# Kernel optimization log

Measured on AMD Instinct MI355X. Metric: run time of the kernel, lower is better.

## Reference

```python
import jax, jax.numpy as jnp
import numpy as np

N_HEAD = 12

def setup_inputs() -> dict:
    key = jax.random.key(0)
    ks = jax.random.split(key, 5)
    B, T, C = 4, 2048, 768
    scale = 0.02
    return {
        "x": jax.random.normal(ks[0], (B, T, C), dtype=jnp.float32),
        "W_attn": jax.random.normal(ks[1], (C, 3 * C), dtype=jnp.float32) * scale,
        "b_attn": jax.random.normal(ks[2], (3 * C,), dtype=jnp.float32) * scale,
        "W_proj": jax.random.normal(ks[3], (C, C), dtype=jnp.float32) * scale,
        "b_proj": jax.random.normal(ks[4], (C,), dtype=jnp.float32) * scale,
    }

def reference(x, W_attn, b_attn, W_proj, b_proj):
    B, T, C = x.shape
    H = N_HEAD
    D = C // H  # head dim
    qkv = x @ W_attn + b_attn  # [B,T,3C]
    q, k, v = jnp.split(qkv, 3, axis=-1)
    # [B,H,T,D]
    q = q.reshape(B, T, H, D).transpose(0, 2, 1, 3)
    k = k.reshape(B, T, H, D).transpose(0, 2, 1, 3)
    v = v.reshape(B, T, H, D).transpose(0, 2, 1, 3)
    scores = jnp.einsum('bhqd,bhkd->bhqk', q, k) / jnp.sqrt(jnp.float32(D))
    causal = jnp.tril(jnp.ones((T, T), dtype=bool))
    scores = jnp.where(causal[None, None, :, :], scores, jnp.float32(-jnp.inf))
    attn = jax.nn.softmax(scores, axis=-1)
    out = jnp.einsum('bhqk,bhkd->bhqd', attn, v)  # [B,H,T,D]
    out = out.transpose(0, 2, 1, 3).reshape(B, T, C)
    return out @ W_proj + b_proj
```

## Files before the change

kernel.cpp:

```cpp
#include <hip/hip_runtime.h>

typedef float f32x4 __attribute__((ext_vector_type(4)));
typedef __bf16 bf16x8 __attribute__((ext_vector_type(8)));
typedef unsigned short u16x8 __attribute__((ext_vector_type(8)));
typedef unsigned short u16x4 __attribute__((ext_vector_type(4)));

#define MFMA16(a, b, c) __builtin_amdgcn_mfma_f32_16x16x32_bf16((a), (b), (c), 0, 0, 0)

__device__ __forceinline__ unsigned short f2bf(float f) {
    __bf16 h = (__bf16)f;
    union { __bf16 h; unsigned short u; } c; c.h = h;
    return c.u;
}

__device__ __forceinline__ void gload_lds16(const unsigned short* g, unsigned short* l) {
    __builtin_amdgcn_global_load_lds(
        (const __attribute__((address_space(1))) unsigned int*)g,
        (__attribute__((address_space(3))) unsigned int*)l, 16, 0, 0);
}

__global__ void k_convert_bf16(const float* __restrict__ in,
                               unsigned short* __restrict__ out, int n) {
    int i = (blockIdx.x * 256 + threadIdx.x) * 4;
    if (i + 3 < n) {
        float4 v = *reinterpret_cast<const float4*>(in + i);
        ushort4 o;
        o.x = f2bf(v.x); o.y = f2bf(v.y); o.z = f2bf(v.z); o.w = f2bf(v.w);
        *reinterpret_cast<ushort4*>(out + i) = o;
    }
}

__global__ void k_transpose_bf16(const float* __restrict__ in,
                                 unsigned short* __restrict__ out, int R, int C) {
    __shared__ unsigned short tile[32][33];
    int bx = blockIdx.x * 32;
    int by = blockIdx.y * 32;
    int tx = threadIdx.x;
    int ty = threadIdx.y;
    #pragma unroll
    for (int i = ty; i < 32; i += 8)
        tile[i][tx] = f2bf(in[(size_t)(by + i) * C + bx + tx]);
    __syncthreads();
    #pragma unroll
    for (int i = ty; i < 32; i += 8)
        out[(size_t)(bx + i) * R + by + tx] = tile[tx][i];
}

template<int EPI>
__global__ __launch_bounds__(512) void k_gemm_bt(
    const unsigned short* __restrict__ A,
    const unsigned short* __restrict__ Bt,
    const float* __restrict__ bias,
    unsigned short* __restrict__ Qo,
    unsigned short* __restrict__ Ko,
    unsigned short* __restrict__ Vto,
    float* __restrict__ Co,
    int K)
{
    __shared__ unsigned short SM[(256 + 128) * 64];
    unsigned short* As = SM;
    unsigned short* Bs = SM + 256 * 64;
    const int nwg = gridDim.x * gridDim.y;
    const int bid0 = blockIdx.y * gridDim.x + blockIdx.x;
    const int logical = (bid0 & 7) * (nwg >> 3) + (bid0 >> 3);
    const int bm = logical / gridDim.x;
    const int bn = logical % gridDim.x;
    const int tid = threadIdx.x;
    const int w = tid >> 6, l = tid & 63;
    const int wm = w >> 1, wn = w & 1;
    const int ln = l & 15, kb = l >> 4;

    f32x4 acc[4][4];
    #pragma unroll
    for (int i = 0; i < 4; ++i)
        #pragma unroll
        for (int j = 0; j < 4; ++j)
            #pragma unroll
            for (int r = 0; r < 4; ++r) acc[i][j][r] = 0.f;

    const unsigned short* Ab = A + (size_t)(bm * 256) * K;
    const unsigned short* Bb = Bt + (size_t)(bn * 128) * K;

    const int srow = tid >> 3;
    const int sslot = tid & 7;
    const int csw = (sslot ^ (srow & 7)) * 8;

    for (int k0 = 0; k0 < K; k0 += 64) {
        #pragma unroll
        for (int j = 0; j < 4; ++j) {
            const int r = j * 64 + srow;
            gload_lds16(&Ab[(size_t)r * K + k0 + csw], &As[r * 64 + sslot * 8]);
        }
        #pragma unroll
        for (int j = 0; j < 2; ++j) {
            const int r = j * 64 + srow;
            gload_lds16(&Bb[(size_t)r * K + k0 + csw], &Bs[r * 64 + sslot * 8]);
        }
        __syncthreads();
        #pragma unroll
        for (int kh = 0; kh < 2; ++kh) {
            bf16x8 af[4], bfr[4];
            #pragma unroll
            for (int mt = 0; mt < 4; ++mt) {
                const int row = wm * 64 + mt * 16 + ln;
                const int slot = ((kh << 2) | kb) ^ (row & 7);
                af[mt] = *reinterpret_cast<const bf16x8*>(&As[row * 64 + slot * 8]);
            }
            #pragma unroll
            for (int nt = 0; nt < 4; ++nt) {
                const int row = wn * 64 + nt * 16 + ln;
                const int slot = ((kh << 2) | kb) ^ (row & 7);
                bfr[nt] = *reinterpret_cast<const bf16x8*>(&Bs[row * 64 + slot * 8]);
            }
            #pragma unroll
            for (int mt = 0; mt < 4; ++mt)
                #pragma unroll
                for (int nt = 0; nt < 4; ++nt)
                    acc[mt][nt] = MFMA16(af[mt], bfr[nt], acc[mt][nt]);
        }
        __syncthreads();
    }

    const float SC = 0.1803368801111204f;

    if (EPI == 0 && bn >= 12) {
        unsigned short* Ts = SM;
        const int cl_w = wn * 64;
        #pragma unroll
        for (int hh2 = 0; hh2 < 2; ++hh2) {
            if ((wm >> 1) == hh2) {
                #pragma unroll
                for (int mt = 0; mt < 4; ++mt) {
                    #pragma unroll
                    for (int nt = 0; nt < 4; ++nt) {
                        const int cl = cl_w + nt * 16 + ln;
                        const float bv = bias[bn * 128 + cl];
                        #pragma unroll
                        for (int r = 0; r < 4; ++r) {
                            const int rl = (wm & 1) * 64 + mt * 16 + kb * 4 + r;
                            const int pos = cl * 128 + ((((rl >> 3) ^ (cl & 7)) << 3) | (rl & 7));
                            Ts[pos] = f2bf(acc[mt][nt][r] + bv);
                        }
                    }
                }
            }
            __syncthreads();
            {
                const int cl = tid >> 2;
                const int col = bn * 128 + cl;
                const int cc = col - 1536;
                const int hh = cc >> 6, dd = cc & 63;
                #pragma unroll
                for (int j8 = 0; j8 < 4; ++j8) {
                    const int rb = (tid & 3) * 4 + j8;
                    u16x8 val = *reinterpret_cast<const u16x8*>(&Ts[cl * 128 + ((rb ^ (cl & 7)) << 3)]);
                    const int tg = bm * 256 + hh2 * 128 + rb * 8;
                    const int bb = tg >> 11;
                    const int tloc = tg & 2047;
                    const int grp = tloc & ~31;
                    const int jj = (tloc >> 3) & 3;
                    const int tlo = grp + 8 * ((2 * jj) & 3) + 4 * (jj >> 1);
                    const int thi = grp + 8 * ((2 * jj + 1) & 3) + 4 * (jj >> 1);
                    unsigned short* basep = &Vto[((size_t)((bb * 12 + hh) * 64 + dd)) * 2048];
                    *reinterpret_cast<u16x4*>(basep + tlo) =
                        __builtin_shufflevector(val, val, 0, 1, 2, 3);
                    *reinterpret_cast<u16x4*>(basep + thi) =
                        __builtin_shufflevector(val, val, 4, 5, 6, 7);
                }
            }
            __syncthreads();
        }
        return;
    }

    #pragma unroll
    for (int mt = 0; mt < 4; ++mt) {
        #pragma unroll
        for (int nt = 0; nt < 4; ++nt) {
            const int col = bn * 128 + wn * 64 + nt * 16 + ln;
            #pragma unroll
            for (int r = 0; r < 4; ++r) {
                const int row = bm * 256 + wm * 64 + mt * 16 + kb * 4 + r;
                float v = acc[mt][nt][r] + bias[col];
                if (EPI == 0) {
                    int cc = col >= 768 ? col - 768 : col;
                    int h = cc >> 6, d = cc & 63;
                    int b = row >> 11, t = row & 2047;
                    if (col < 768)
                        Qo[((size_t)((b * 12 + h) * 2048 + t)) * 64 + d] = f2bf(v * SC);
                    else
                        Ko[((size_t)((b * 12 + h) * 2048 + t)) * 64 + d] = f2bf(v);
                } else {
                    Co[(size_t)row * 768 + col] = v;
                }
            }
        }
    }
}

__global__ __launch_bounds__(256) void k_attn(
    const unsigned short* __restrict__ Q,
    const unsigned short* __restrict__ Kk,
    const unsigned short* __restrict__ Vt,
    unsigned short* __restrict__ Oo)
{
    __shared__ unsigned short SMEM[4 * 4096];
    const int bid0 = blockIdx.x;
    const int xcd = bid0 & 7;
    const int loc = bid0 >> 3;
    const int qb = 15 - (loc / 6);
    const int bh = xcd * 6 + (loc % 6);
    const int tid = threadIdx.x;
    const int w = tid >> 6, l = tid & 63;
    const int ln = l & 15, kb = l >> 4;
    const int kbq = kb * 4;
    const int b = bh / 12, h = bh - b * 12;
    const int q0w = qb * 128 + w * 32;

    const unsigned short* Qb = Q + (size_t)bh * 2048 * 64;
    const unsigned short* Kb = Kk + (size_t)bh * 2048 * 64;
    const unsigned short* Vb = Vt + (size_t)bh * 64 * 2048;

    bf16x8 qf[2][2];
    #pragma unroll
    for (int qn = 0; qn < 2; ++qn) {
        const unsigned short* qr = &Qb[(size_t)(q0w + qn * 16 + ln) * 64 + kb * 8];
        qf[qn][0] = *reinterpret_cast<const bf16x8*>(qr);
        qf[qn][1] = *reinterpret_cast<const bf16x8*>(qr + 32);
    }

    bf16x8 vones;
    #pragma unroll
    for (int e = 0; e < 8; ++e) vones[e] = (__bf16)1.0f;
    const f32x4 fzero = {0.f, 0.f, 0.f, 0.f};

    f32x4 oaccT[2][4];
    f32x4 den[2];
    #pragma unroll
    for (int qn = 0; qn < 2; ++qn) {
        #pragma unroll
        for (int r = 0; r < 4; ++r) den[qn][r] = 0.f;
        #pragma unroll
        for (int dt = 0; dt < 4; ++dt)
            #pragma unroll
            for (int r = 0; r < 4; ++r) oaccT[qn][dt][r] = 0.f;
    }

    const int lb = ln & 7;
    const int aR0 = ln * 64 + (kb ^ lb) * 8;
    const int aR1 = ln * 64 + ((4 | kb) ^ lb) * 8;

    const int srow = tid >> 3;
    const int sslot = tid & 7;
    const int csw = (sslot ^ (srow & 7)) * 8;
    const int ntile = 2 * qb + 2;
    const int lastkt = (q0w + 31) >> 6;

    #define STAGE(kt_, buf_)                                                        \
        {                                                                           \
            const int kb_ = (kt_) * 64;                                             \
            _Pragma("unroll")                                                       \
            for (int j = 0; j < 2; ++j) {                                           \
                const int r = j * 32 + srow;                                        \
                gload_lds16(&Kb[(size_t)(kb_ + r) * 64 + csw],                      \
                            &SMEM[(buf_) * 4096 + r * 64 + sslot * 8]);             \
                gload_lds16(&Vb[(size_t)r * 2048 + kb_ + csw],                      \
                            &SMEM[8192 + (buf_) * 4096 + r * 64 + sslot * 8]);      \
            }                                                                       \
        }

    #define COMPUTE(kt_, BUF)                                                       \
        if ((kt_) <= lastkt) {                                                      \
            bf16x8 kf[4][2];                                                        \
            _Pragma("unroll")                                                       \
            for (int km = 0; km < 4; ++km) {                                        \
                kf[km][0] = *reinterpret_cast<const bf16x8*>(                       \
                    &SMEM[(BUF) * 4096 + km * 1024 + aR0]);                         \
                kf[km][1] = *reinterpret_cast<const bf16x8*>(                       \
                    &SMEM[(BUF) * 4096 + km * 1024 + aR1]);                         \
            }                                                                       \
            f32x4 st[4][2];                                                         \
            _Pragma("unroll")                                                       \
            for (int km = 0; km < 4; ++km)                                          \
                _Pragma("unroll")                                                   \
                for (int qn = 0; qn < 2; ++qn) {                                    \
                    st[km][qn] = MFMA16(kf[km][0], qf[qn][0], fzero);               \
                    st[km][qn] = MFMA16(kf[km][1], qf[qn][1], st[km][qn]);          \
                }                                                                   \
            bf16x8 vf[4][2];                                                        \
            _Pragma("unroll")                                                       \
            for (int dt = 0; dt < 4; ++dt) {                                        \
                vf[dt][0] = *reinterpret_cast<const bf16x8*>(                       \
                    &SMEM[8192 + (BUF) * 4096 + dt * 1024 + aR0]);                  \
                vf[dt][1] = *reinterpret_cast<const bf16x8*>(                       \
                    &SMEM[8192 + (BUF) * 4096 + dt * 1024 + aR1]);                  \
            }                                                                       \
            if ((kt_) == lastkt) {                                                  \
                const int kbase_ = (kt_) * 64;                                      \
                _Pragma("unroll")                                                   \
                for (int qn = 0; qn < 2; ++qn) {                                    \
                    const int qrow = q0w + qn * 16 + ln;                            \
                    _Pragma("unroll")                                               \
                    for (int km = 0; km < 4; ++km)                                  \
                        _Pragma("unroll")                                           \
                        for (int r = 0; r < 4; ++r) {                               \
                            float sv = st[km][qn][r];                               \
                            const int key = kbase_ + km * 16 + kbq + r;             \
                            sv = (key <= qrow) ? sv : -1e30f;                       \
                            st[km][qn][r] = __builtin_amdgcn_exp2f(sv);             \
                        }                                                           \
                }                                                                   \
            } else {                                                                \
                _Pragma("unroll")                                                   \
                for (int qn = 0; qn < 2; ++qn)                                      \
                    _Pragma("unroll")                                               \
                    for (int km = 0; km < 4; ++km)                                  \
                        _Pragma("unroll")                                           \
                        for (int r = 0; r < 4; ++r)                                 \
                            st[km][qn][r] =                                         \
                                __builtin_amdgcn_exp2f(st[km][qn][r]);              \
            }                                                                       \
            bf16x8 pa[2][2];                                                        \
            _Pragma("unroll")                                                       \
            for (int qn = 0; qn < 2; ++qn)                                          \
                _Pragma("unroll")                                                   \
                for (int kh = 0; kh < 2; ++kh) {                                    \
                    bf16x8 t;                                                       \
                    _Pragma("unroll")                                               \
                    for (int r = 0; r < 4; ++r) {                                   \
                        t[r]     = (__bf16)st[2 * kh][qn][r];                       \
                        t[r + 4] = (__bf16)st[2 * kh + 1][qn][r];                   \
                    }                                                               \
                    pa[qn][kh] = t;                                                 \
                }                                                                   \
            _Pragma("unroll")                                                       \
            for (int qn = 0; qn < 2; ++qn) {                                        \
                _Pragma("unroll")                                                   \
                for (int dt = 0; dt < 4; ++dt) {                                    \
                    oaccT[qn][dt] = MFMA16(pa[qn][0], vf[dt][0], oaccT[qn][dt]);    \
                    oaccT[qn][dt] = MFMA16(pa[qn][1], vf[dt][1], oaccT[qn][dt]);    \
                }                                                                   \
                den[qn] = MFMA16(pa[qn][0], vones, den[qn]);                        \
                den[qn] = MFMA16(pa[qn][1], vones, den[qn]);                        \
            }                                                                       \
        }

    STAGE(0, 0);

    for (int s = 0; s <= qb; ++s) {
        const int ktA = 2 * s;
        const int ktB = 2 * s + 1;
        __syncthreads();
        STAGE(ktB, 1);
        COMPUTE(ktA, 0);
        __syncthreads();
        if (s < qb) STAGE(ktA + 2, 0);
        COMPUTE(ktB, 1);
    }

    #pragma unroll
    for (int qn = 0; qn < 2; ++qn) {
        #pragma unroll
        for (int r = 0; r < 4; ++r) {
            const float inv = 1.0f / den[qn][r];
            const int t = q0w + qn * 16 + kbq + r;
            #pragma unroll
            for (int dt = 0; dt < 4; ++dt)
                Oo[((size_t)(b * 2048 + t)) * 768 + h * 64 + dt * 16 + ln] =
                    f2bf(oaccT[qn][dt][r] * inv);
        }
    }
    #undef STAGE
    #undef COMPUTE
}

extern "C" void kernel_launch(void* const* d_in, const int* in_sizes, int n_in,
                              void* d_out, int out_size, void* d_ws, size_t ws_size,
                              hipStream_t stream) {
    const float* x      = (const float*)d_in[0];
    const float* W_attn = (const float*)d_in[1];
    const float* b_attn = (const float*)d_in[2];
    const float* W_proj = (const float*)d_in[3];
    const float* b_proj = (const float*)d_in[4];
    float* out = (float*)d_out;

    char* ws = (char*)d_ws;
    const size_t SZ_X  = (size_t)8192 * 768 * 2;
    const size_t SZ_WA = (size_t)2304 * 768 * 2;
    const size_t SZ_WP = (size_t)768 * 768 * 2;
    const size_t SZ_T  = (size_t)8192 * 768 * 2;

    unsigned short* x_bf = (unsigned short*)(ws);
    unsigned short* wa_t = (unsigned short*)(ws + SZ_X);
    unsigned short* wp_t = (unsigned short*)(ws + SZ_X + SZ_WA);
    unsigned short* Qb   = (unsigned short*)(ws + SZ_X + SZ_WA + SZ_WP);
    unsigned short* Kb   = (unsigned short*)(ws + SZ_X + SZ_WA + SZ_WP + SZ_T);
    unsigned short* Vtb  = (unsigned short*)(ws + SZ_X + SZ_WA + SZ_WP + 2 * SZ_T);
    unsigned short* attn_o = x_bf;

    k_convert_bf16<<<6144, 256, 0, stream>>>(x, x_bf, 8192 * 768);
    dim3 tb(32, 8);
    k_transpose_bf16<<<dim3(2304 / 32, 768 / 32), tb, 0, stream>>>(W_attn, wa_t, 768, 2304);
    k_transpose_bf16<<<dim3(768 / 32, 768 / 32), tb, 0, stream>>>(W_proj, wp_t, 768, 768);
    k_gemm_bt<0><<<dim3(18, 32), 512, 0, stream>>>(x_bf, wa_t, b_attn, Qb, Kb, Vtb, nullptr, 768);
    k_attn<<<768, 256, 0, stream>>>(Qb, Kb, Vtb, attn_o);
    k_gemm_bt<1><<<dim3(6, 32), 512, 0, stream>>>(attn_o, wp_t, b_proj, nullptr, nullptr, nullptr, out, 768);
}
```

Before: 121.0 us.

## Triple-buffer QKV GEMM pipeline and split projection GEMM into smaller tiles

The QKV GEMM now uses a three-stage LDS ring with K-step 32. It issues loads two steps ahead and waits on partial vmcnt, so global loads overlap the MFMA work instead of being fenced by a full sync every iteration. The output projection becomes its own kernel with 128x128 tiles and 256 threads over a 6x64 grid, which doubles the number of workgroups for the small GEMM. This costs more LDS per QKV block and adds hand-written waitcnt and barrier scheduling that must match the load counts exactly.

```diff
diff --git a/kernel.cpp b/kernel.cpp
--- a/kernel.cpp
+++ b/kernel.cpp
@@ -46,20 +46,16 @@
         out[(size_t)(bx + i) * R + by + tx] = tile[tx][i];
 }
 
-template<int EPI>
-__global__ __launch_bounds__(512) void k_gemm_bt(
+__global__ __launch_bounds__(512) void k_gemm_qkv(
     const unsigned short* __restrict__ A,
     const unsigned short* __restrict__ Bt,
     const float* __restrict__ bias,
     unsigned short* __restrict__ Qo,
     unsigned short* __restrict__ Ko,
     unsigned short* __restrict__ Vto,
-    float* __restrict__ Co,
     int K)
 {
-    __shared__ unsigned short SM[(256 + 128) * 64];
-    unsigned short* As = SM;
-    unsigned short* Bs = SM + 256 * 64;
+    __shared__ unsigned short SM[3 * 8192 + 3 * 4096];
     const int nwg = gridDim.x * gridDim.y;
     const int bid0 = blockIdx.y * gridDim.x + blockIdx.x;
     const int logical = (bid0 & 7) * (nwg >> 3) + (bid0 >> 3);
@@ -81,49 +77,60 @@
     const unsigned short* Ab = A + (size_t)(bm * 256) * K;
     const unsigned short* Bb = Bt + (size_t)(bn * 128) * K;
 
-    const int srow = tid >> 3;
-    const int sslot = tid & 7;
-    const int csw = (sslot ^ (srow & 7)) * 8;
-
-    for (int k0 = 0; k0 < K; k0 += 64) {
-        #pragma unroll
-        for (int j = 0; j < 4; ++j) {
-            const int r = j * 64 + srow;
-            gload_lds16(&Ab[(size_t)r * K + k0 + csw], &As[r * 64 + sslot * 8]);
-        }
-        #pragma unroll
-        for (int j = 0; j < 2; ++j) {
-            const int r = j * 64 + srow;
-            gload_lds16(&Bb[(size_t)r * K + k0 + csw], &Bs[r * 64 + sslot * 8]);
-        }
-        __syncthreads();
-        #pragma unroll
-        for (int kh = 0; kh < 2; ++kh) {
-            bf16x8 af[4], bfr[4];
-            #pragma unroll
-            for (int mt = 0; mt < 4; ++mt) {
-                const int row = wm * 64 + mt * 16 + ln;
-                const int slot = ((kh << 2) | kb) ^ (row & 7);
-                af[mt] = *reinterpret_cast<const bf16x8*>(&As[row * 64 + slot * 8]);
-            }
-            #pragma unroll
-            for (int nt = 0; nt < 4; ++nt) {
-                const int row = wn * 64 + nt * 16 + ln;
-                const int slot = ((kh << 2) | kb) ^ (row & 7);
-                bfr[nt] = *reinterpret_cast<const bf16x8*>(&Bs[row * 64 + slot * 8]);
-            }
-            #pragma unroll
-            for (int mt = 0; mt < 4; ++mt)
-                #pragma unroll
-                for (int nt = 0; nt < 4; ++nt)
-                    acc[mt][nt] = MFMA16(af[mt], bfr[nt], acc[mt][nt]);
-        }
-        __syncthreads();
-    }
+    const int srow = tid >> 2;
+    const int sslot = tid & 3;
+    const int scs = (sslot ^ ((srow >> 1) & 3)) * 8;
+    const int slot8 = (kb ^ ((ln >> 1) & 3)) * 8;
+    const int aOff = (wm * 64 + ln) * 32 + slot8;
+    const int bOff = 24576 + (wn * 64 + ln) * 32 + slot8;
+
+    #define QSTAGE(t_, buf_)                                                        \
+        {                                                                           \
+            const int k0_ = (t_) * 32;                                              \
+            gload_lds16(&Ab[(size_t)srow * K + k0_ + scs],                          \
+                        &SM[(buf_) * 8192 + srow * 32 + sslot * 8]);                \
+            gload_lds16(&Ab[(size_t)(128 + srow) * K + k0_ + scs],                  \
+                        &SM[(buf_) * 8192 + (128 + srow) * 32 + sslot * 8]);        \
+            gload_lds16(&Bb[(size_t)srow * K + k0_ + scs],                          \
+                        &SM[24576 + (buf_) * 4096 + srow * 32 + sslot * 8]);        \
+        }
+
+    #define QSTEP(t_, BUF_, NBUF_)                                                  \
+        {                                                                           \
+            if ((t_) < 23) { asm volatile("s_waitcnt vmcnt(3)" ::: "memory"); }     \
+            else           { asm volatile("s_waitcnt vmcnt(0)" ::: "memory"); }     \
+            __builtin_amdgcn_sched_barrier(0);                                      \
+            __builtin_amdgcn_s_barrier();                                           \
+            if ((t_) + 2 < 24) QSTAGE((t_) + 2, NBUF_);                             \
+            bf16x8 af[4], bfr[4];                                                   \
+            _Pragma("unroll")                                                       \
+            for (int mt = 0; mt < 4; ++mt)                                          \
+                af[mt] = *reinterpret_cast<const bf16x8*>(                          \
+                    &SM[(BUF_) * 8192 + mt * 512 + aOff]);                          \
+            _Pragma("unroll")                                                       \
+            for (int nt = 0; nt < 4; ++nt)                                          \
+                bfr[nt] = *reinterpret_cast<const bf16x8*>(                         \
+                    &SM[(BUF_) * 4096 + nt * 512 + bOff]);                          \
+            _Pragma("unroll")                                                       \
+            for (int mt = 0; mt < 4; ++mt)                                          \
+                _Pragma("unroll")                                                   \
+                for (int nt = 0; nt < 4; ++nt)                                      \
+                    acc[mt][nt] = MFMA16(af[mt], bfr[nt], acc[mt][nt]);             \
+        }
+
+    QSTAGE(0, 0);
+    QSTAGE(1, 1);
+    #pragma unroll
+    for (int s = 0; s < 8; ++s) {
+        QSTEP(3 * s,     0, 2);
+        QSTEP(3 * s + 1, 1, 0);
+        QSTEP(3 * s + 2, 2, 1);
+    }
+    __syncthreads();
 
     const float SC = 0.1803368801111204f;
 
-    if (EPI == 0 && bn >= 12) {
+    if (bn >= 12) {
         unsigned short* Ts = SM;
         const int cl_w = wn * 64;
         #pragma unroll
@@ -182,17 +189,101 @@
             for (int r = 0; r < 4; ++r) {
                 const int row = bm * 256 + wm * 64 + mt * 16 + kb * 4 + r;
                 float v = acc[mt][nt][r] + bias[col];
-                if (EPI == 0) {
-                    int cc = col >= 768 ? col - 768 : col;
-                    int h = cc >> 6, d = cc & 63;
-                    int b = row >> 11, t = row & 2047;
-                    if (col < 768)
-                        Qo[((size_t)((b * 12 + h) * 2048 + t)) * 64 + d] = f2bf(v * SC);
-                    else
-                        Ko[((size_t)((b * 12 + h) * 2048 + t)) * 64 + d] = f2bf(v);
-                } else {
-                    Co[(size_t)row * 768 + col] = v;
-                }
+                int cc = col >= 768 ? col - 768 : col;
+                int h = cc >> 6, d = cc & 63;
+                int b = row >> 11, t = row & 2047;
+                if (col < 768)
+                    Qo[((size_t)((b * 12 + h) * 2048 + t)) * 64 + d] = f2bf(v * SC);
+                else
+                    Ko[((size_t)((b * 12 + h) * 2048 + t)) * 64 + d] = f2bf(v);
+            }
+        }
+    }
+    #undef QSTAGE
+    #undef QSTEP
+}
+
+__global__ __launch_bounds__(256) void k_gemm_proj(
+    const unsigned short* __restrict__ A,
+    const unsigned short* __restrict__ Bt,
+    const float* __restrict__ bias,
+    float* __restrict__ Co,
+    int K)
+{
+    constexpr int BM = 128;
+    __shared__ unsigned short SM[(BM + 128) * 64];
+    unsigned short* As = SM;
+    unsigned short* Bs = SM + BM * 64;
+    const int nwg = gridDim.x * gridDim.y;
+    const int bid0 = blockIdx.y * gridDim.x + blockIdx.x;
+    const int logical = (bid0 & 7) * (nwg >> 3) + (bid0 >> 3);
+    const int bm = logical / gridDim.x;
+    const int bn = logical % gridDim.x;
+    const int tid = threadIdx.x;
+    const int w = tid >> 6, l = tid & 63;
+    const int wm = w >> 1, wn = w & 1;
+    const int ln = l & 15, kb = l >> 4;
+
+    f32x4 acc[4][4];
+    #pragma unroll
+    for (int i = 0; i < 4; ++i)
+        #pragma unroll
+        for (int j = 0; j < 4; ++j)
+            #pragma unroll
+            for (int r = 0; r < 4; ++r) acc[i][j][r] = 0.f;
+
+    const unsigned short* Ab = A + (size_t)(bm * BM) * K;
+    const unsigned short* Bb = Bt + (size_t)(bn * 128) * K;
+
+    const int srow = tid >> 3;
+    const int sslot = tid & 7;
+    const int csw = (sslot ^ (srow & 7)) * 8;
+
+    for (int k0 = 0; k0 < K; k0 += 64) {
+        #pragma unroll
+        for (int j = 0; j < 4; ++j) {
+            const int r = j * 32 + srow;
+            gload_lds16(&Ab[(size_t)r * K + k0 + csw], &As[r * 64 + sslot * 8]);
+        }
+        #pragma unroll
+        for (int j = 0; j < 4; ++j) {
+            const int r = j * 32 + srow;
+            gload_lds16(&Bb[(size_t)r * K + k0 + csw], &Bs[r * 64 + sslot * 8]);
+        }
+        __syncthreads();
+        #pragma unroll
+        for (int kh = 0; kh < 2; ++kh) {
+            bf16x8 af[4], bfr[4];
+            #pragma unroll
+            for (int mt = 0; mt < 4; ++mt) {
+                const int row = wm * 64 + mt * 16 + ln;
+                const int slot = ((kh << 2) | kb) ^ (row & 7);
+                af[mt] = *reinterpret_cast<const bf16x8*>(&As[row * 64 + slot * 8]);
+            }
+            #pragma unroll
+            for (int nt = 0; nt < 4; ++nt) {
+                const int row = wn * 64 + nt * 16 + ln;
+                const int slot = ((kh << 2) | kb) ^ (row & 7);
+                bfr[nt] = *reinterpret_cast<const bf16x8*>(&Bs[row * 64 + slot * 8]);
+            }
+            #pragma unroll
+            for (int mt = 0; mt < 4; ++mt)
+                #pragma unroll
+                for (int nt = 0; nt < 4; ++nt)
+                    acc[mt][nt] = MFMA16(af[mt], bfr[nt], acc[mt][nt]);
+        }
+        __syncthreads();
+    }
+
+    #pragma unroll
+    for (int mt = 0; mt < 4; ++mt) {
+        #pragma unroll
+        for (int nt = 0; nt < 4; ++nt) {
+            const int col = bn * 128 + wn * 64 + nt * 16 + ln;
+            #pragma unroll
+            for (int r = 0; r < 4; ++r) {
+                const int row = bm * BM + wm * 64 + mt * 16 + kb * 4 + r;
+                Co[(size_t)row * 768 + col] = acc[mt][nt][r] + bias[col];
             }
         }
     }
@@ -253,7 +344,6 @@
     const int srow = tid >> 3;
     const int sslot = tid & 7;
     const int csw = (sslot ^ (srow & 7)) * 8;
-    const int ntile = 2 * qb + 2;
     const int lastkt = (q0w + 31) >> 6;
 
     #define STAGE(kt_, buf_)                                                        \
@@ -402,7 +492,7 @@
     dim3 tb(32, 8);
     k_transpose_bf16<<<dim3(2304 / 32, 768 / 32), tb, 0, stream>>>(W_attn, wa_t, 768, 2304);
     k_transpose_bf16<<<dim3(768 / 32, 768 / 32), tb, 0, stream>>>(W_proj, wp_t, 768, 768);
-    k_gemm_bt<0><<<dim3(18, 32), 512, 0, stream>>>(x_bf, wa_t, b_attn, Qb, Kb, Vtb, nullptr, 768);
+    k_gemm_qkv<<<dim3(18, 32), 512, 0, stream>>>(x_bf, wa_t, b_attn, Qb, Kb, Vtb, 768);
     k_attn<<<768, 256, 0, stream>>>(Qb, Kb, Vtb, attn_o);
-    k_gemm_bt<1><<<dim3(6, 32), 512, 0, stream>>>(attn_o, wp_t, b_proj, nullptr, nullptr, nullptr, out, 768);
-}
+    k_gemm_proj<<<dim3(6, 64), 256, 0, stream>>>(attn_o, wp_t, b_proj, out, 768);
+}
```

Measured after the change: 117.5 us. 1.03x faster.
